# Kernel optimization log

Hardware: AMD Instinct MI355X
Metric: run time of the kernel (lower is better)

## Reference

```python
import jax, jax.numpy as jnp
import numpy as np

FRACTAL_OUTPUT = (5, 5)            # (a, b); requires 5 * num_kernels == a*b
PERC_THRESHOLD = 0.59275
NEXT_SHAPE = (224, 224)
K_END = int(0.4 * FRACTAL_OUTPUT[0] * FRACTAL_OUTPUT[1] + 1)   # 11
KERNEL_SIZES = list(range(3, K_END + 1, 2))                    # [3,5,7,9,11]


def setup_inputs() -> dict:
    key = jax.random.key(0)
    inputs = jax.random.uniform(key, (64, 224, 224, 3), dtype=jnp.float32) * 255.0
    return {"inputs": inputs}


def _extract_patches(x, k):
    # tf.image.extract_patches(sizes=strides=k, SAME) == zero-pad + space-to-depth
    B, H, W, C = x.shape
    rows, cols = -(-H // k), -(-W // k)
    ph, pw = rows * k - H, cols * k - W
    x = jnp.pad(x, ((0, 0), (ph // 2, ph - ph // 2), (pw // 2, pw - pw // 2), (0, 0)))
    x = x.reshape(B, rows, k, cols, k, C).transpose(0, 1, 3, 2, 4, 5)
    return x.reshape(B * rows * cols, k, k, C), rows * cols


def _binarize(patches, k, ch):
    # distance function: 1 iff |channel value - center pixel channel value| <= k
    center = patches[:, k // 2, k // 2, ch][:, None, None]
    return (jnp.abs(patches[..., ch] - center) <= k).astype(jnp.int32)


def _connected_stats(binp, k):
    # 4-connected components via min-label propagation (== tfa connected_components
    # up to relabeling; we only need #components and max label count incl. background)
    N = binp.shape[0]
    idx = jnp.arange(1, k * k + 1, dtype=jnp.int32).reshape(k, k)
    INF = jnp.int32(k * k + 2)
    lbl0 = jnp.where(binp > 0, idx, 0)

    def step(_, lbl):
        v = jnp.where(binp > 0, lbl, INF)
        pad = lambda a, w: jnp.pad(a, ((0, 0),) + w, constant_values=INF)
        up    = pad(v, ((1, 0), (0, 0)))[:, :-1, :]
        down  = pad(v, ((0, 1), (0, 0)))[:, 1:, :]
        left  = pad(v, ((0, 0), (1, 0)))[:, :, :-1]
        right = pad(v, ((0, 0), (0, 1)))[:, :, 1:]
        m = jnp.minimum(jnp.minimum(v, up), jnp.minimum(jnp.minimum(down, left), right))
        return jnp.where(binp > 0, m, 0)

    lbl = jax.lax.fori_loop(0, k * k, step, lbl0)  # k*k iters guarantee convergence
    ncomp = jnp.sum((binp > 0) & (lbl == idx), axis=(1, 2)).astype(jnp.int32)
    lblf = lbl.reshape(N, k * k)
    cnt = jnp.zeros((N, k * k + 1), jnp.int32).at[jnp.arange(N)[:, None], lblf].add(1)
    return ncomp, cnt.max(axis=1)  # (#components, most-common label count incl bg 0)


def _components(inputs, k, ch):
    B = inputs.shape[0]
    patches, P = _extract_patches(inputs, k)
    binp = _binarize(patches, k, ch)                    # (B*P, k, k)
    ones = binp.sum(axis=(1, 2)).reshape(B, P)          # int counts per patch
    # tf.bincount(minlength=1, maxlength=k*k): bins 0..k*k-1, value k*k dropped
    cnt = jnp.zeros((B, k * k + 1), jnp.float32).at[jnp.arange(B)[:, None], ones].add(1.0)
    prob = cnt[:, : k * k] / P                          # (B, k*k)
    n = jnp.arange(1, k * k + 1, dtype=jnp.float32)
    fd = (prob / n).sum(1)
    m = (prob * n).sum(1)
    m2 = ((prob * prob) * n).sum(1)
    lac = (m2 - m * m) / (m * m)
    perc = ((ones.astype(jnp.float32) / (k * k)) >= PERC_THRESHOLD).astype(jnp.int32)
    acp = perc.sum(1) // P                              # tf integer reduce_mean
    ncomp, marea = _connected_stats(binp, k)
    acn = ncomp.reshape(B, P).sum(1) // P
    acma = marea.reshape(B, P).sum(1) // P
    return jnp.stack([acn.astype(jnp.float32), acp.astype(jnp.float32),
                      acma.astype(jnp.float32), lac, fd], axis=1)   # (B, 5)


def _rearrange(c):
    # group metric-major: all acn over kernels, then acp, acma, lac, fd
    return jnp.concatenate([c[:, mm::5] for mm in range(5)], axis=1)


def reference(inputs):
    B = inputs.shape[0]
    chans = []
    for ch in range(3):
        comps = jnp.concatenate([_components(inputs, k, ch) for k in KERNEL_SIZES], axis=1)
        chans.append(_rearrange(comps).reshape(B, FRACTAL_OUTPUT[0], FRACTAL_OUTPUT[1]))
    out = jnp.stack(chans, axis=3)                      # (B, a, b, 3)
    return jax.image.resize(out, (B, NEXT_SHAPE[0], NEXT_SHAPE[1], 3), method='bilinear')
```

## Files before the change

kernel.cpp:

```cpp
#include <hip/hip_runtime.h>

#define HW 224
#define NIMG 64
#define NPIX ((size_t)NIMG * HW * HW)
#define ACC_STRIDE 128
#define NCOMBO (NIMG * 15)
#define ACC_BYTES (NCOMBO * ACC_STRIDE * 4)

typedef unsigned long long u64;

struct U128 { u64 lo, hi; };

__device__ __forceinline__ u64  u_or  (u64 a, u64 b){ return a | b; }
__device__ __forceinline__ u64  u_and (u64 a, u64 b){ return a & b; }
__device__ __forceinline__ u64  u_andn(u64 a, u64 b){ return a & ~b; }
__device__ __forceinline__ bool u_eq(u64 a, u64 b){ return a == b; }
__device__ __forceinline__ bool u_nz(u64 a){ return a != 0ull; }
__device__ __forceinline__ u64  u_shl(u64 a, int n){ return a << n; }
__device__ __forceinline__ u64  u_shr(u64 a, int n){ return a >> n; }
__device__ __forceinline__ int  u_pop(u64 a){ return __popcll(a); }
__device__ __forceinline__ u64  u_low(u64 a){ return a & (0ull - a); }

__device__ __forceinline__ U128 u_or  (U128 a, U128 b){ return {a.lo|b.lo, a.hi|b.hi}; }
__device__ __forceinline__ U128 u_and (U128 a, U128 b){ return {a.lo&b.lo, a.hi&b.hi}; }
__device__ __forceinline__ U128 u_andn(U128 a, U128 b){ return {a.lo&~b.lo, a.hi&~b.hi}; }
__device__ __forceinline__ bool u_eq(U128 a, U128 b){ return a.lo==b.lo && a.hi==b.hi; }
__device__ __forceinline__ bool u_nz(U128 a){ return (a.lo | a.hi) != 0ull; }
__device__ __forceinline__ U128 u_shl(U128 a, int n){
    return { a.lo << n, (a.hi << n) | (a.lo >> (64 - n)) };
}
__device__ __forceinline__ U128 u_shr(U128 a, int n){
    return { (a.lo >> n) | (a.hi << (64 - n)), a.hi >> n };
}
__device__ __forceinline__ int u_pop(U128 a){ return __popcll(a.lo) + __popcll(a.hi); }
__device__ __forceinline__ U128 u_low(U128 a){
    if (a.lo) return { a.lo & (0ull - a.lo), 0ull };
    return { 0ull, a.hi & (0ull - a.hi) };
}

template<bool B, class T, class F> struct sel        { using type = T; };
template<class T, class F>         struct sel<false, T, F> { using type = F; };

template<int K>
__device__ __forceinline__ void load_row(const float* __restrict__ p, float* r) {
#pragma unroll
    for (int j = 0; j + 4 <= K; j += 4) {
        float4 v; __builtin_memcpy(&v, p + j, 16);
        r[j] = v.x; r[j + 1] = v.y; r[j + 2] = v.z; r[j + 3] = v.w;
    }
    if constexpr ((K & 3) >= 2) {
        constexpr int b = (K / 4) * 4;
        float2 v; __builtin_memcpy(&v, p + b, 8);
        r[b] = v.x; r[b + 1] = v.y;
    }
    if constexpr (K & 1) r[K - 1] = p[K - 1];
}

template<int K, int S, class M>
__device__ __forceinline__ void do_patch(const float* __restrict__ img, int p,
                                         M leftCol, M rightCol,
                                         int* bins, int& t_perc, int& t_ncomp,
                                         int& t_marea) {
    constexpr int KK   = K * K;
    constexpr int ROWS = (HW + K - 1) / K;
    constexpr int PAD  = (ROWS * K - HW) / 2;

    const int pr = p / ROWS, pc = p - pr * ROWS;
    const int y0 = pr * K - PAD, x0 = pc * K - PAD;
    const float cen = img[((size_t)(y0 + K / 2) * HW + (x0 + K / 2)) * S];

    M msk;
    if constexpr (KK <= 64) msk = 0ull; else msk = U128{0, 0};

    const bool fast = (S == 1) && (y0 >= 0) && (x0 >= 0) &&
                      (y0 + K <= HW) && (x0 + K <= HW);
    if (fast) {
#pragma unroll
        for (int i = 0; i < K; i++) {
            float r[K];
            load_row<K>(img + (size_t)(y0 + i) * HW + x0, r);
#pragma unroll
            for (int j = 0; j < K; j++) {
                const u64 bit = (fabsf(r[j] - cen) <= (float)K) ? 1ull : 0ull;
                const int cb = i * K + j;
                if constexpr (KK <= 64) msk |= bit << cb;
                else { if (cb < 64) msk.lo |= bit << cb; else msk.hi |= bit << (cb - 64); }
            }
        }
    } else {
#pragma unroll
        for (int i = 0; i < K; i++) {
            const int y = y0 + i;
            const bool yin = (unsigned)y < (unsigned)HW;
#pragma unroll
            for (int j = 0; j < K; j++) {
                const int x = x0 + j;
                const bool inb = yin && ((unsigned)x < (unsigned)HW);
                const float v = inb ? img[((size_t)y * HW + x) * S] : 0.0f;
                const u64 bit = (fabsf(v - cen) <= (float)K) ? 1ull : 0ull;
                const int cb = i * K + j;
                if constexpr (KK <= 64) msk |= bit << cb;
                else { if (cb < 64) msk.lo |= bit << cb; else msk.hi |= bit << (cb - 64); }
            }
        }
    }
    const int ones = u_pop(msk);

    M nbm = u_or(u_or(u_shl(u_andn(msk, rightCol), 1),
                      u_shr(u_andn(msk, leftCol ), 1)),
                 u_or(u_shl(msk, K), u_shr(msk, K)));
    M iso = u_andn(msk, nbm);
    const int niso = u_pop(iso);
    int ncomp = niso, maxsz = (niso > 0) ? 1 : 0;
    M m = u_andn(msk, iso);
    while (u_nz(m)) {
        M s = u_low(m);
        for (;;) {
            M g = u_or(s, u_or(u_or(u_shl(u_andn(s, rightCol), 1),
                                    u_shr(u_andn(s, leftCol ), 1)),
                               u_or(u_shl(s, K), u_shr(s, K))));
            g = u_and(g, m);
            if (u_eq(g, s)) break;
            s = g;
        }
        ncomp++;
        const int sz = u_pop(s);
        if (sz > maxsz) maxsz = sz;
        m = u_andn(m, s);
    }

    const int bgcnt = KK - ones;
    const int marea = (bgcnt > maxsz) ? bgcnt : maxsz;
    t_ncomp += ncomp;
    t_marea += marea;
    if ((float)ones / (float)KK >= 0.59275f) t_perc++;
    atomicAdd(&bins[ones], 1);
}

template<int K>
__device__ __forceinline__ void make_colmasks(u64& lcl, u64& lch, u64& rcl, u64& rch) {
    lcl = lch = rcl = rch = 0;
#pragma unroll
    for (int i = 0; i < K; i++) {
        const int cl = i * K, cr = i * K + K - 1;
        if (cl < 64) lcl |= 1ull << cl; else lch |= 1ull << (cl - 64);
        if (cr < 64) rcl |= 1ull << cr; else rch |= 1ull << (cr - 64);
    }
}

template<int K, int S>
__device__ __forceinline__ void job_body(const float* __restrict__ img,
                                         int chunk, int lane, int* hist,
                                         int* __restrict__ gout) {
    constexpr int ROWS = (HW + K - 1) / K;
    constexpr int P    = ROWS * ROWS;
    constexpr int PPJ  = (K == 3) ? 512 : (K == 5 ? 128 : 64);
    constexpr int KK   = K * K;
    using M = typename sel<(KK <= 64), u64, U128>::type;

    u64 lcl, lch, rcl, rch;
    make_colmasks<K>(lcl, lch, rcl, rch);
    M leftCol, rightCol;
    if constexpr (KK <= 64) { leftCol = lcl; rightCol = rcl; }
    else { leftCol = U128{lcl, lch}; rightCol = U128{rcl, rch}; }

    for (int s = lane; s <= KK; s += 64) hist[s] = 0;

    const int pstart = chunk * PPJ;
    const int pend   = (pstart + PPJ < P) ? (pstart + PPJ) : P;

    int t_perc = 0, t_ncomp = 0, t_marea = 0;
    for (int p = pstart + lane; p < pend; p += 64)
        do_patch<K, S, M>(img, p, leftCol, rightCol, hist,
                          t_perc, t_ncomp, t_marea);

#pragma unroll
    for (int off = 32; off; off >>= 1) {
        t_perc  += __shfl_down(t_perc,  off);
        t_ncomp += __shfl_down(t_ncomp, off);
        t_marea += __shfl_down(t_marea, off);
    }
    if (lane == 0) {
        atomicAdd(&gout[124], t_perc);
        atomicAdd(&gout[125], t_ncomp);
        atomicAdd(&gout[126], t_marea);
    }
    for (int s = lane; s <= KK; s += 64) {
        const int v = hist[s];
        if (v) atomicAdd(&gout[s], v);
    }
}

template<int S>
__global__ __launch_bounds__(256) void fractal_stats(const float* __restrict__ in,
                                                     int* __restrict__ gacc) {
    const int wave = threadIdx.x >> 6;
    const int lane = threadIdx.x & 63;
    const int x    = blockIdx.x & 7;
    const int j    = blockIdx.x >> 3;
    const int gl   = j / 15, ib = j - gl * 15;
    const int g    = gl * 8 + x;
    const int b    = g / 3, ch = g - b * 3;
    const int jw   = ib * 4 + wave;

    __shared__ int hist[4][124];

    int kidx, chunk;
    if      (jw < 7)  { kidx = 4; chunk = jw;      }
    else if (jw < 17) { kidx = 3; chunk = jw - 7;  }
    else if (jw < 28) { kidx = 0; chunk = jw - 17; }
    else if (jw < 44) { kidx = 1; chunk = jw - 28; }
    else              { kidx = 2; chunk = jw - 44; }

    const float* img = (S == 1) ? in + ((size_t)ch * NIMG + b) * HW * HW
                                : in + (size_t)b * HW * HW * 3 + ch;
    int* gout = gacc + (g * 5 + kidx) * ACC_STRIDE;

    switch (kidx) {
        case 0: job_body<3,  S>(img, chunk, lane, hist[wave], gout); break;
        case 1: job_body<5,  S>(img, chunk, lane, hist[wave], gout); break;
        case 2: job_body<7,  S>(img, chunk, lane, hist[wave], gout); break;
        case 3: job_body<9,  S>(img, chunk, lane, hist[wave], gout); break;
        case 4: job_body<11, S>(img, chunk, lane, hist[wave], gout); break;
    }
}

__global__ __launch_bounds__(64) void fractal_finalize(const int* __restrict__ gacc,
                                                       float* __restrict__ interm) {
    const int cidx = blockIdx.x * 64 + threadIdx.x;
    if (cidx >= NCOMBO) return;
    const int b    = cidx / 15;
    const int rem  = cidx % 15;
    const int ch   = rem / 5;
    const int kidx = rem % 5;
    const int K    = 3 + 2 * kidx;
    const int ROWS = (HW + K - 1) / K;
    const int P    = ROWS * ROWS;
    const int KK   = K * K;

    const int* a = gacc + cidx * ACC_STRIDE;
    const float Pf = (float)P;
    float fd = 0.0f, m1 = 0.0f, m2 = 0.0f;
    for (int s = 0; s < KK; s++) {
        const float prob = (float)a[s] / Pf;
        const float n = (float)(s + 1);
        fd += prob / n;
        m1 += prob * n;
        m2 += prob * prob * n;
    }
    const float lac = (m2 - m1 * m1) / (m1 * m1);

    float* o = interm + (size_t)b * 75 + kidx * 3 + ch;
    o[0]  = (float)(a[125] / P);
    o[15] = (float)(a[124] / P);
    o[30] = (float)(a[126] / P);
    o[45] = lac;
    o[60] = fd;
}

template<int K, int S>
__device__ __forceinline__ void stats_body_full(const float* __restrict__ img,
                                                float* __restrict__ o,
                                                int hist4[4][124], int* sums) {
    constexpr int KK   = K * K;
    constexpr int ROWS = (HW + K - 1) / K;
    constexpr int P    = ROWS * ROWS;
    using M = typename sel<(KK <= 64), u64, U128>::type;
    const int wid = threadIdx.x >> 6;

    u64 lcl, lch, rcl, rch;
    make_colmasks<K>(lcl, lch, rcl, rch);
    M leftCol, rightCol;
    if constexpr (KK <= 64) { leftCol = lcl; rightCol = rcl; }
    else { leftCol = U128{lcl, lch}; rightCol = U128{rcl, rch}; }

    int t_perc = 0, t_ncomp = 0, t_marea = 0;
    for (int p = threadIdx.x; p < P; p += 256)
        do_patch<K, S, M>(img, p, leftCol, rightCol, hist4[wid],
                          t_perc, t_ncomp, t_marea);

    atomicAdd(&sums[0], t_perc);
    atomicAdd(&sums[1], t_ncomp);
    atomicAdd(&sums[2], t_marea);
    __syncthreads();

    if (threadIdx.x == 0) {
        const float Pf = (float)P;
        float fd = 0.0f, m1 = 0.0f, m2 = 0.0f;
        for (int s = 0; s < KK; s++) {
            const float prob = (float)(hist4[0][s] + hist4[1][s] + hist4[2][s] + hist4[3][s]) / Pf;
            const float n = (float)(s + 1);
            fd += prob / n;
            m1 += prob * n;
            m2 += prob * prob * n;
        }
        const float lac = (m2 - m1 * m1) / (m1 * m1);
        o[0]  = (float)(sums[1] / P);
        o[15] = (float)(sums[0] / P);
        o[30] = (float)(sums[2] / P);
        o[45] = lac;
        o[60] = fd;
    }
}

template<int S>
__global__ __launch_bounds__(256) void fractal_stats_full(const float* __restrict__ in,
                                                          float* __restrict__ interm) {
    const int b    = blockIdx.x / 15;
    const int rem  = blockIdx.x % 15;
    const int ch   = rem / 5;
    const int kidx = rem % 5;

    __shared__ int hist[4][124];
    __shared__ int sums[3];
    for (int i = threadIdx.x; i < 4 * 124; i += 256) ((int*)hist)[i] = 0;
    if (threadIdx.x < 3) sums[threadIdx.x] = 0;
    __syncthreads();

    const float* img = in + (size_t)b * HW * HW * 3 + ch;
    float* o = interm + (size_t)b * 75 + kidx * 3 + ch;

    switch (kidx) {
        case 0: stats_body_full<3,  S>(img, o, hist, sums); break;
        case 1: stats_body_full<5,  S>(img, o, hist, sums); break;
        case 2: stats_body_full<7,  S>(img, o, hist, sums); break;
        case 3: stats_body_full<9,  S>(img, o, hist, sums); break;
        case 4: stats_body_full<11, S>(img, o, hist, sums); break;
    }
}

__global__ __launch_bounds__(256) void deinterleave(const float* __restrict__ in,
                                                    float* __restrict__ planes,
                                                    int* __restrict__ gacc) {
    const int t = blockIdx.x * 256 + threadIdx.x;
    if (t < ACC_BYTES / 16) {
        const int4 z = make_int4(0, 0, 0, 0);
        ((int4*)gacc)[t] = z;
    }
    const size_t pix = (size_t)t * 4;
    if (pix >= NPIX) return;
    float4 a, b, c;
    __builtin_memcpy(&a, in + pix * 3,     16);
    __builtin_memcpy(&b, in + pix * 3 + 4, 16);
    __builtin_memcpy(&c, in + pix * 3 + 8, 16);
    const float4 p0 = make_float4(a.x, a.w, b.z, c.y);
    const float4 p1 = make_float4(a.y, b.x, b.w, c.z);
    const float4 p2 = make_float4(a.z, b.y, c.x, c.w);
    __builtin_memcpy(planes + pix,            &p0, 16);
    __builtin_memcpy(planes + NPIX + pix,     &p1, 16);
    __builtin_memcpy(planes + 2 * NPIX + pix, &p2, 16);
}

__global__ __launch_bounds__(256) void fractal_resize(const float* __restrict__ interm,
                                                      float* __restrict__ out, int total) {
    const int x = threadIdx.x;
    if (x >= HW) return;
    const int y = blockIdx.x, b = blockIdx.y;

    const float sc = 5.0f / 224.0f;
    const float uy = ((float)y + 0.5f) * sc - 0.5f;
    const float ux = ((float)x + 0.5f) * sc - 0.5f;

    const float fy = floorf(uy), fx = floorf(ux);
    const float wy = uy - fy,    wx = ux - fx;
    int y0 = (int)fy, x0 = (int)fx;
    int y1 = y0 + 1,  x1 = x0 + 1;
    if (y0 < 0) y0 = 0; if (x0 < 0) x0 = 0;
    if (y1 > 4) y1 = 4; if (x1 > 4) x1 = 4;

    const float w00 = (1.0f - wy) * (1.0f - wx), w01 = (1.0f - wy) * wx;
    const float w10 = wy * (1.0f - wx),          w11 = wy * wx;

    const float* gp = interm + (size_t)b * 75;
    const int base = ((b * HW + y) * HW + x) * 3;
    if (base + 3 > total) return;
#pragma unroll
    for (int ch = 0; ch < 3; ch++) {
        out[base + ch] = w00 * gp[(y0 * 5 + x0) * 3 + ch]
                       + w01 * gp[(y0 * 5 + x1) * 3 + ch]
                       + w10 * gp[(y1 * 5 + x0) * 3 + ch]
                       + w11 * gp[(y1 * 5 + x1) * 3 + ch];
    }
}

extern "C" void kernel_launch(void* const* d_in, const int* in_sizes, int n_in,
                              void* d_out, int out_size, void* d_ws, size_t ws_size,
                              hipStream_t stream) {
    const float* in = (const float*)d_in[0];
    float* out = (float*)d_out;
    float* interm = (float*)d_ws;

    const size_t acc_off    = 19456;
    const size_t planes_off = acc_off + ACC_BYTES;
    const size_t need = planes_off + 3 * NPIX * sizeof(float);

    if (ws_size >= need) {
        int*   gacc   = (int*)((char*)d_ws + acc_off);
        float* planes = (float*)((char*)d_ws + planes_off);
        deinterleave<<<(int)(NPIX / 4 / 256), 256, 0, stream>>>(in, planes, gacc);
        fractal_stats<1><<<2880, 256, 0, stream>>>(planes, gacc);
        fractal_finalize<<<(NCOMBO + 63) / 64, 64, 0, stream>>>(gacc, interm);
    } else {
        fractal_stats_full<3><<<NIMG * 15, 256, 0, stream>>>(in, interm);
    }
    fractal_resize<<<dim3(HW, NIMG), 256, 0, stream>>>(interm, out, out_size);
}
```

Measured before the change: 166.7 us.

## Fuse finalize into resize, rebalance stats work into uniform 64-thread slices

The separate finalize kernel is removed: every resize block now recomputes the 15 per-image statistics from the accumulators into shared memory, which saves one launch but repeats the finalize arithmetic in each of the 224 row blocks. The stats kernel moves from 256-thread blocks with a hand-tuned uneven chunk mapping to 64-thread blocks, each covering one eighth of the patches for one kernel size. For K<=9 the whole patch is loaded into registers before comparison, taking the center from registers instead of a separate global load, and the K<=5 loop is unrolled by 2. These changes raise register pressure and change the load balance across blocks.

Measured after the change: 268.9 us. 61.3% more time.

```diff
diff --git a/kernel.cpp b/kernel.cpp
--- a/kernel.cpp
+++ b/kernel.cpp
@@ -3,6 +3,7 @@
 #define HW 224
 #define NIMG 64
 #define NPIX ((size_t)NIMG * HW * HW)
+#define NSLICE 8
 #define ACC_STRIDE 128
 #define NCOMBO (NIMG * 15)
 #define ACC_BYTES (NCOMBO * ACC_STRIDE * 4)
@@ -67,7 +68,6 @@
 
     const int pr = p / ROWS, pc = p - pr * ROWS;
     const int y0 = pr * K - PAD, x0 = pc * K - PAD;
-    const float cen = img[((size_t)(y0 + K / 2) * HW + (x0 + K / 2)) * S];
 
     M msk;
     if constexpr (KK <= 64) msk = 0ull; else msk = U128{0, 0};
@@ -75,19 +75,39 @@
     const bool fast = (S == 1) && (y0 >= 0) && (x0 >= 0) &&
                       (y0 + K <= HW) && (x0 + K <= HW);
     if (fast) {
-#pragma unroll
-        for (int i = 0; i < K; i++) {
-            float r[K];
-            load_row<K>(img + (size_t)(y0 + i) * HW + x0, r);
-#pragma unroll
-            for (int j = 0; j < K; j++) {
-                const u64 bit = (fabsf(r[j] - cen) <= (float)K) ? 1ull : 0ull;
-                const int cb = i * K + j;
-                if constexpr (KK <= 64) msk |= bit << cb;
-                else { if (cb < 64) msk.lo |= bit << cb; else msk.hi |= bit << (cb - 64); }
+        if constexpr (K <= 9) {
+            float r[K][K];
+#pragma unroll
+            for (int i = 0; i < K; i++)
+                load_row<K>(img + (size_t)(y0 + i) * HW + x0, r[i]);
+            const float cen = r[K / 2][K / 2];
+#pragma unroll
+            for (int i = 0; i < K; i++) {
+#pragma unroll
+                for (int j = 0; j < K; j++) {
+                    const u64 bit = (fabsf(r[i][j] - cen) <= (float)K) ? 1ull : 0ull;
+                    const int cb = i * K + j;
+                    if constexpr (KK <= 64) msk |= bit << cb;
+                    else { if (cb < 64) msk.lo |= bit << cb; else msk.hi |= bit << (cb - 64); }
+                }
+            }
+        } else {
+            const float cen = img[(size_t)(y0 + K / 2) * HW + (x0 + K / 2)];
+#pragma unroll
+            for (int i = 0; i < K; i++) {
+                float r[K];
+                load_row<K>(img + (size_t)(y0 + i) * HW + x0, r);
+#pragma unroll
+                for (int j = 0; j < K; j++) {
+                    const u64 bit = (fabsf(r[j] - cen) <= (float)K) ? 1ull : 0ull;
+                    const int cb = i * K + j;
+                    if constexpr (KK <= 64) msk |= bit << cb;
+                    else { if (cb < 64) msk.lo |= bit << cb; else msk.hi |= bit << (cb - 64); }
+                }
             }
         }
     } else {
+        const float cen = img[((size_t)(y0 + K / 2) * HW + (x0 + K / 2)) * S];
 #pragma unroll
         for (int i = 0; i < K; i++) {
             const int y = y0 + i;
@@ -150,11 +170,10 @@
 
 template<int K, int S>
 __device__ __forceinline__ void job_body(const float* __restrict__ img,
-                                         int chunk, int lane, int* hist,
+                                         int slice, int lane, int* hist,
                                          int* __restrict__ gout) {
     constexpr int ROWS = (HW + K - 1) / K;
     constexpr int P    = ROWS * ROWS;
-    constexpr int PPJ  = (K == 3) ? 512 : (K == 5 ? 128 : 64);
     constexpr int KK   = K * K;
     using M = typename sel<(KK <= 64), u64, U128>::type;
 
@@ -166,13 +185,20 @@
 
     for (int s = lane; s <= KK; s += 64) hist[s] = 0;
 
-    const int pstart = chunk * PPJ;
-    const int pend   = (pstart + PPJ < P) ? (pstart + PPJ) : P;
+    const int pstart = (slice * P) / NSLICE;
+    const int pend   = ((slice + 1) * P) / NSLICE;
 
     int t_perc = 0, t_ncomp = 0, t_marea = 0;
-    for (int p = pstart + lane; p < pend; p += 64)
-        do_patch<K, S, M>(img, p, leftCol, rightCol, hist,
-                          t_perc, t_ncomp, t_marea);
+    if constexpr (K <= 5) {
+#pragma unroll 2
+        for (int p = pstart + lane; p < pend; p += 64)
+            do_patch<K, S, M>(img, p, leftCol, rightCol, hist,
+                              t_perc, t_ncomp, t_marea);
+    } else {
+        for (int p = pstart + lane; p < pend; p += 64)
+            do_patch<K, S, M>(img, p, leftCol, rightCol, hist,
+                              t_perc, t_ncomp, t_marea);
+    }
 
 #pragma unroll
     for (int off = 32; off; off >>= 1) {
@@ -192,70 +218,93 @@
 }
 
 template<int S>
-__global__ __launch_bounds__(256) void fractal_stats(const float* __restrict__ in,
-                                                     int* __restrict__ gacc) {
-    const int wave = threadIdx.x >> 6;
-    const int lane = threadIdx.x & 63;
-    const int x    = blockIdx.x & 7;
-    const int j    = blockIdx.x >> 3;
-    const int gl   = j / 15, ib = j - gl * 15;
-    const int g    = gl * 8 + x;
-    const int b    = g / 3, ch = g - b * 3;
-    const int jw   = ib * 4 + wave;
-
-    __shared__ int hist[4][124];
-
-    int kidx, chunk;
-    if      (jw < 7)  { kidx = 4; chunk = jw;      }
-    else if (jw < 17) { kidx = 3; chunk = jw - 7;  }
-    else if (jw < 28) { kidx = 0; chunk = jw - 17; }
-    else if (jw < 44) { kidx = 1; chunk = jw - 28; }
-    else              { kidx = 2; chunk = jw - 44; }
+__global__ __launch_bounds__(64) void fractal_stats(const float* __restrict__ in,
+                                                    int* __restrict__ gacc) {
+    const int B     = blockIdx.x;
+    const int x     = B & 7;
+    const int j     = B >> 3;
+    const int gl    = j / 40;
+    const int inner = j - gl * 40;
+    const int g     = gl * 8 + x;
+    const int b     = g / 3, ch = g - b * 3;
+    const int kidx  = inner >> 3;
+    const int slice = inner & 7;
+
+    __shared__ int hist[124];
 
     const float* img = (S == 1) ? in + ((size_t)ch * NIMG + b) * HW * HW
                                 : in + (size_t)b * HW * HW * 3 + ch;
     int* gout = gacc + (g * 5 + kidx) * ACC_STRIDE;
 
     switch (kidx) {
-        case 0: job_body<3,  S>(img, chunk, lane, hist[wave], gout); break;
-        case 1: job_body<5,  S>(img, chunk, lane, hist[wave], gout); break;
-        case 2: job_body<7,  S>(img, chunk, lane, hist[wave], gout); break;
-        case 3: job_body<9,  S>(img, chunk, lane, hist[wave], gout); break;
-        case 4: job_body<11, S>(img, chunk, lane, hist[wave], gout); break;
-    }
-}
-
-__global__ __launch_bounds__(64) void fractal_finalize(const int* __restrict__ gacc,
-                                                       float* __restrict__ interm) {
-    const int cidx = blockIdx.x * 64 + threadIdx.x;
-    if (cidx >= NCOMBO) return;
-    const int b    = cidx / 15;
-    const int rem  = cidx % 15;
-    const int ch   = rem / 5;
-    const int kidx = rem % 5;
-    const int K    = 3 + 2 * kidx;
-    const int ROWS = (HW + K - 1) / K;
-    const int P    = ROWS * ROWS;
-    const int KK   = K * K;
-
-    const int* a = gacc + cidx * ACC_STRIDE;
-    const float Pf = (float)P;
-    float fd = 0.0f, m1 = 0.0f, m2 = 0.0f;
-    for (int s = 0; s < KK; s++) {
-        const float prob = (float)a[s] / Pf;
-        const float n = (float)(s + 1);
-        fd += prob / n;
-        m1 += prob * n;
-        m2 += prob * prob * n;
-    }
-    const float lac = (m2 - m1 * m1) / (m1 * m1);
-
-    float* o = interm + (size_t)b * 75 + kidx * 3 + ch;
-    o[0]  = (float)(a[125] / P);
-    o[15] = (float)(a[124] / P);
-    o[30] = (float)(a[126] / P);
-    o[45] = lac;
-    o[60] = fd;
+        case 0: job_body<3,  S>(img, slice, threadIdx.x, hist, gout); break;
+        case 1: job_body<5,  S>(img, slice, threadIdx.x, hist, gout); break;
+        case 2: job_body<7,  S>(img, slice, threadIdx.x, hist, gout); break;
+        case 3: job_body<9,  S>(img, slice, threadIdx.x, hist, gout); break;
+        case 4: job_body<11, S>(img, slice, threadIdx.x, hist, gout); break;
+    }
+}
+
+__global__ __launch_bounds__(256) void fractal_resize_acc(const int* __restrict__ gacc,
+                                                          float* __restrict__ out,
+                                                          int total) {
+    const int y = blockIdx.x, b = blockIdx.y;
+    __shared__ float vals[75];
+
+    if (threadIdx.x < 15) {
+        const int rem  = threadIdx.x;
+        const int ch   = rem / 5;
+        const int kidx = rem % 5;
+        const int K    = 3 + 2 * kidx;
+        const int ROWS = (HW + K - 1) / K;
+        const int P    = ROWS * ROWS;
+        const int KK   = K * K;
+
+        const int* a = gacc + (b * 15 + rem) * ACC_STRIDE;
+        const float Pf = (float)P;
+        float fd = 0.0f, m1 = 0.0f, m2 = 0.0f;
+        for (int s = 0; s < KK; s++) {
+            const float prob = (float)a[s] / Pf;
+            const float n = (float)(s + 1);
+            fd += prob / n;
+            m1 += prob * n;
+            m2 += prob * prob * n;
+        }
+        const float lac = (m2 - m1 * m1) / (m1 * m1);
+        vals[(0 * 5 + kidx) * 3 + ch] = (float)(a[125] / P);
+        vals[(1 * 5 + kidx) * 3 + ch] = (float)(a[124] / P);
+        vals[(2 * 5 + kidx) * 3 + ch] = (float)(a[126] / P);
+        vals[(3 * 5 + kidx) * 3 + ch] = lac;
+        vals[(4 * 5 + kidx) * 3 + ch] = fd;
+    }
+    __syncthreads();
+
+    const int x = threadIdx.x;
+    if (x >= HW) return;
+
+    const float sc = 5.0f / 224.0f;
+    const float uy = ((float)y + 0.5f) * sc - 0.5f;
+    const float ux = ((float)x + 0.5f) * sc - 0.5f;
+
+    const float fy = floorf(uy), fx = floorf(ux);
+    const float wy = uy - fy,    wx = ux - fx;
+    int y0 = (int)fy, x0 = (int)fx;
+    int y1 = y0 + 1,  x1 = x0 + 1;
+    if (y0 < 0) y0 = 0; if (x0 < 0) x0 = 0;
+    if (y1 > 4) y1 = 4; if (x1 > 4) x1 = 4;
+
+    const float w00 = (1.0f - wy) * (1.0f - wx), w01 = (1.0f - wy) * wx;
+    const float w10 = wy * (1.0f - wx),          w11 = wy * wx;
+
+    const int base = ((b * HW + y) * HW + x) * 3;
+    if (base + 3 > total) return;
+#pragma unroll
+    for (int ch = 0; ch < 3; ch++) {
+        out[base + ch] = w00 * vals[(y0 * 5 + x0) * 3 + ch]
+                       + w01 * vals[(y0 * 5 + x1) * 3 + ch]
+                       + w10 * vals[(y1 * 5 + x0) * 3 + ch]
+                       + w11 * vals[(y1 * 5 + x1) * 3 + ch];
+    }
 }
 
 template<int K, int S>
@@ -329,6 +378,38 @@
     }
 }
 
+__global__ __launch_bounds__(256) void fractal_resize(const float* __restrict__ interm,
+                                                      float* __restrict__ out, int total) {
+    const int x = threadIdx.x;
+    if (x >= HW) return;
+    const int y = blockIdx.x, b = blockIdx.y;
+
+    const float sc = 5.0f / 224.0f;
+    const float uy = ((float)y + 0.5f) * sc - 0.5f;
+    const float ux = ((float)x + 0.5f) * sc - 0.5f;
+
+    const float fy = floorf(uy), fx = floorf(ux);
+    const float wy = uy - fy,    wx = ux - fx;
+    int y0 = (int)fy, x0 = (int)fx;
+    int y1 = y0 + 1,  x1 = x0 + 1;
+    if (y0 < 0) y0 = 0; if (x0 < 0) x0 = 0;
+    if (y1 > 4) y1 = 4; if (x1 > 4) x1 = 4;
+
+    const float w00 = (1.0f - wy) * (1.0f - wx), w01 = (1.0f - wy) * wx;
+    const float w10 = wy * (1.0f - wx),          w11 = wy * wx;
+
+    const float* gp = interm + (size_t)b * 75;
+    const int base = ((b * HW + y) * HW + x) * 3;
+    if (base + 3 > total) return;
+#pragma unroll
+    for (int ch = 0; ch < 3; ch++) {
+        out[base + ch] = w00 * gp[(y0 * 5 + x0) * 3 + ch]
+                       + w01 * gp[(y0 * 5 + x1) * 3 + ch]
+                       + w10 * gp[(y1 * 5 + x0) * 3 + ch]
+                       + w11 * gp[(y1 * 5 + x1) * 3 + ch];
+    }
+}
+
 __global__ __launch_bounds__(256) void deinterleave(const float* __restrict__ in,
                                                     float* __restrict__ planes,
                                                     int* __restrict__ gacc) {
@@ -351,38 +432,6 @@
     __builtin_memcpy(planes + 2 * NPIX + pix, &p2, 16);
 }
 
-__global__ __launch_bounds__(256) void fractal_resize(const float* __restrict__ interm,
-                                                      float* __restrict__ out, int total) {
-    const int x = threadIdx.x;
-    if (x >= HW) return;
-    const int y = blockIdx.x, b = blockIdx.y;
-
-    const float sc = 5.0f / 224.0f;
-    const float uy = ((float)y + 0.5f) * sc - 0.5f;
-    const float ux = ((float)x + 0.5f) * sc - 0.5f;
-
-    const float fy = floorf(uy), fx = floorf(ux);
-    const float wy = uy - fy,    wx = ux - fx;
-    int y0 = (int)fy, x0 = (int)fx;
-    int y1 = y0 + 1,  x1 = x0 + 1;
-    if (y0 < 0) y0 = 0; if (x0 < 0) x0 = 0;
-    if (y1 > 4) y1 = 4; if (x1 > 4) x1 = 4;
-
-    const float w00 = (1.0f - wy) * (1.0f - wx), w01 = (1.0f - wy) * wx;
-    const float w10 = wy * (1.0f - wx),          w11 = wy * wx;
-
-    const float* gp = interm + (size_t)b * 75;
-    const int base = ((b * HW + y) * HW + x) * 3;
-    if (base + 3 > total) return;
-#pragma unroll
-    for (int ch = 0; ch < 3; ch++) {
-        out[base + ch] = w00 * gp[(y0 * 5 + x0) * 3 + ch]
-                       + w01 * gp[(y0 * 5 + x1) * 3 + ch]
-                       + w10 * gp[(y1 * 5 + x0) * 3 + ch]
-                       + w11 * gp[(y1 * 5 + x1) * 3 + ch];
-    }
-}
-
 extern "C" void kernel_launch(void* const* d_in, const int* in_sizes, int n_in,
                               void* d_out, int out_size, void* d_ws, size_t ws_size,
                               hipStream_t stream) {
@@ -398,10 +447,10 @@
         int*   gacc   = (int*)((char*)d_ws + acc_off);
         float* planes = (float*)((char*)d_ws + planes_off);
         deinterleave<<<(int)(NPIX / 4 / 256), 256, 0, stream>>>(in, planes, gacc);
-        fractal_stats<1><<<2880, 256, 0, stream>>>(planes, gacc);
-        fractal_finalize<<<(NCOMBO + 63) / 64, 64, 0, stream>>>(gacc, interm);
+        fractal_stats<1><<<192 * 40, 64, 0, stream>>>(planes, gacc);
+        fractal_resize_acc<<<dim3(HW, NIMG), 256, 0, stream>>>(gacc, out, out_size);
     } else {
         fractal_stats_full<3><<<NIMG * 15, 256, 0, stream>>>(in, interm);
-    }
-    fractal_resize<<<dim3(HW, NIMG), 256, 0, stream>>>(interm, out, out_size);
-}
+        fractal_resize<<<dim3(HW, NIMG), 256, 0, stream>>>(interm, out, out_size);
+    }
+}
```
